# Performance work log

Measured on AMD Instinct MI355X. Metric: run time of the kernel, lower is better.

The kernel has to match this reference:

```python
import jax, jax.numpy as jnp
import numpy as np

N_NODES = 100000
N_EDGES = 1600000
VOCAB = 1000
D_IN = 64
D_H = 128
D_OUT = 1
NEG_SLOPE = 0.2  # PyG GATConv default leaky_relu slope


def setup_inputs() -> dict:
    key = jax.random.key(0)
    ks = jax.random.split(key, 13)
    s_in = 1.0 / np.sqrt(D_IN)
    s_h = 1.0 / np.sqrt(D_H)
    return {
        "x": jax.random.randint(ks[0], (N_NODES,), 0, VOCAB),
        "edge_index": jax.random.randint(ks[1], (2, N_EDGES), 0, N_NODES),
        "node_embeddings": jax.random.normal(ks[2], (VOCAB, D_IN)) * 0.1,
        "W1": jax.random.normal(ks[3], (D_IN, D_H)) * s_in,
        "a_src1": jax.random.normal(ks[4], (D_H,)) * s_h,
        "a_dst1": jax.random.normal(ks[5], (D_H,)) * s_h,
        "b1": jnp.zeros((D_H,)),
        "W2": jax.random.normal(ks[6], (D_H, D_H)) * s_h,
        "a_src2": jax.random.normal(ks[7], (D_H,)) * s_h,
        "a_dst2": jax.random.normal(ks[8], (D_H,)) * s_h,
        "b2": jnp.zeros((D_H,)),
        "W_fc": jax.random.normal(ks[9], (2 * D_H, D_OUT)) * (1.0 / np.sqrt(2 * D_H)),
        "b_fc": jnp.zeros((D_OUT,)),
    }


def segment_softmax(logits, seg, n):
    # numerically-stable softmax over edges grouped by destination node
    mx = jax.ops.segment_max(logits, seg, num_segments=n)
    e = jnp.exp(logits - mx[seg])
    s = jax.ops.segment_sum(e, seg, num_segments=n)
    return e / (s[seg] + 1e-16)


def gat_conv(h, src, dst, W, a_src, a_dst, b):
    # single-head GATConv (PyG defaults: heads=1, negative_slope=0.2, bias)
    h = h @ W                                   # [N, D]
    logit = (h @ a_src)[src] + (h @ a_dst)[dst]  # [E]
    logit = jax.nn.leaky_relu(logit, NEG_SLOPE)
    alpha = segment_softmax(logit, dst, N_NODES)
    out = jax.ops.segment_sum(alpha[:, None] * h[src], dst, num_segments=N_NODES)
    return out + b


def reference(x, edge_index, node_embeddings, W1, a_src1, a_dst1, b1,
              W2, a_src2, a_dst2, b2, W_fc, b_fc):
    h = node_embeddings[x]                      # [N, D_IN]
    src, dst = edge_index[0], edge_index[1]
    # PyG GATConv adds self-loops by default
    loop = jnp.arange(N_NODES)
    src_sl = jnp.concatenate([src, loop])
    dst_sl = jnp.concatenate([dst, loop])
    h = jax.nn.gelu(gat_conv(h, src_sl, dst_sl, W1, a_src1, a_dst1, b1), approximate=False)
    h = jax.nn.gelu(gat_conv(h, src_sl, dst_sl, W2, a_src2, a_dst2, b2), approximate=False)
    # per-edge prediction: concat endpoint features (original edges, no self-loops)
    pair = jnp.concatenate([h[src], h[dst]], axis=-1)   # [E, 2*D_H]
    out = jax.nn.gelu(pair @ W_fc + b_fc, approximate=False)
    return out.squeeze(1)                       # [E]
```

## Files before the change

kernel.cpp:

```cpp
#include <hip/hip_runtime.h>
#include <hip/hip_bf16.h>

#define N_NODES 100000
#define N_EDGES 1600000
#define N_ESL   1700000
#define VOCAB   1000
#define D_IN    64
#define D_H     128
#define NEG_SLOPE 0.2f

#define BSH   7
#define NB    782
#define CAP   3072
#define CHUNK 16384

#define CO_EMB   0
#define CO_W1    64000
#define CO_AS1   72192
#define CO_AD1   72320
#define CO_B1    72448
#define CO_W2    72576
#define CO_AS2   88960
#define CO_AD2   89088
#define CO_B2    89216
#define CO_WFC   89344
#define CO_BFC   89600
#define CO_TOTAL 89601

__device__ __forceinline__ float us2f(unsigned short h){ union{unsigned v; float f;} c; c.v = ((unsigned)h)<<16; return c.f; }
__device__ __forceinline__ float gelu_f(float v){ return 0.5f*v*(1.0f + erff(v*0.7071067811865475f)); }
__device__ __forceinline__ float4 ldf4(const float* p){ return *reinterpret_cast<const float4*>(p); }
__device__ __forceinline__ void stf4(float* p, float4 v){ *reinterpret_cast<float4*>(p) = v; }

__device__ __forceinline__ float wred_sum(float v){
  #pragma unroll
  for (int m=32;m;m>>=1) v += __shfl_xor(v,m,64);
  return v;
}

__global__ __launch_bounds__(64) void k_detect(const unsigned* __restrict__ w, int* __restrict__ flag){
  int t = threadIdx.x;
  float cnt = 0.f;
  #pragma unroll
  for (int i=0;i<2;++i){
    unsigned v = w[t + 64*i];
    unsigned e = (v >> 7) & 0xFFu;
    cnt += (e >= 110u && e <= 126u) ? 1.f : 0.f;
  }
  cnt = wred_sum(cnt);
  if (t==0) *flag = (cnt >= 64.f) ? 1 : 0;
}

__global__ void k_convert(const void* p0, const void* p1, const void* p2, const void* p3,
    const void* p4, const void* p5, const void* p6, const void* p7, const void* p8,
    const void* p9, const void* p10, const int* __restrict__ flag, float* __restrict__ c){
  int i = blockIdx.x*blockDim.x + threadIdx.x;
  if (i >= CO_TOTAL) return;
  const void* src; int off;
  if      (i < CO_W1 ){ src=p0;  off=i;          }
  else if (i < CO_AS1){ src=p1;  off=i-CO_W1;    }
  else if (i < CO_AD1){ src=p2;  off=i-CO_AS1;   }
  else if (i < CO_B1 ){ src=p3;  off=i-CO_AD1;   }
  else if (i < CO_W2 ){ src=p4;  off=i-CO_B1;    }
  else if (i < CO_AS2){ src=p5;  off=i-CO_W2;    }
  else if (i < CO_AD2){ src=p6;  off=i-CO_AS2;   }
  else if (i < CO_B2 ){ src=p7;  off=i-CO_AD2;   }
  else if (i < CO_WFC){ src=p8;  off=i-CO_B2;    }
  else if (i < CO_BFC){ src=p9;  off=i-CO_WFC;   }
  else               { src=p10; off=i-CO_BFC;   }
  float v = (*flag) ? us2f(((const unsigned short*)src)[off]) : ((const float*)src)[off];
  c[i] = v;
}

__global__ __launch_bounds__(256) void k_prevec(const float* __restrict__ cw,
    float* __restrict__ va2, float* __restrict__ vd2){
  int t = threadIdx.x;
  int r = t & 127;
  const float* vec = cw + ((t < 128) ? CO_AS2 : CO_AD2);
  float s = 0.f;
  for (int j=0;j<D_H;++j) s = fmaf(cw[CO_W2 + r*D_H + j], vec[j], s);
  if (t < 128) va2[r] = s; else vd2[r] = s;
}

__global__ __launch_bounds__(64) void k_table1(const float* __restrict__ cw,
    float* __restrict__ table1, float* __restrict__ as1, float* __restrict__ ad1){
  const float* emb = cw + CO_EMB;
  const float* W1  = cw + CO_W1;
  int v = blockIdx.x; int t = threadIdx.x;
  __shared__ float er[D_IN];
  er[t] = emb[v*D_IN + t];
  __syncthreads();
  int d0 = t, d1 = t + 64;
  float a0 = 0.f, a1 = 0.f;
  for (int k=0;k<D_IN;++k){
    float e = er[k];
    a0 = fmaf(e, W1[k*D_H+d0], a0);
    a1 = fmaf(e, W1[k*D_H+d1], a1);
  }
  table1[v*D_H+d0] = a0; table1[v*D_H+d1] = a1;
  float ps = a0*cw[CO_AS1+d0] + a1*cw[CO_AS1+d1];
  float pd = a0*cw[CO_AD1+d0] + a1*cw[CO_AD1+d1];
  ps = wred_sum(ps); pd = wred_sum(pd);
  if (t==0){ as1[v]=ps; ad1[v]=pd; }
}

__global__ void k_nodelog(const int* __restrict__ x, const float* __restrict__ as1,
    const float* __restrict__ ad1, float* __restrict__ sA1, float* __restrict__ dA1){
  int i = blockIdx.x*blockDim.x + threadIdx.x;
  if (i < N_NODES){ int xs = x[i]; sA1[i] = as1[xs]; dA1[i] = ad1[xs]; }
}

__global__ __launch_bounds__(256) void k_bin(const int* __restrict__ src,
    const int* __restrict__ dst, int* __restrict__ gcur, unsigned* __restrict__ ebuf){
  __shared__ int hist[NB];
  __shared__ int cur[NB];
  int tid = threadIdx.x;
  int base0 = blockIdx.x * CHUNK;
  int n = N_ESL - base0; if (n > CHUNK) n = CHUNK;
  for (int i=tid; i<NB; i+=256) hist[i] = 0;
  __syncthreads();
  for (int k=tid; k<n; k+=256){
    int e = base0 + k;
    int d = (e < N_EDGES) ? dst[e] : (e - N_EDGES);
    atomicAdd(&hist[d>>BSH], 1);
  }
  __syncthreads();
  for (int b=tid; b<NB; b+=256){
    int c = hist[b];
    cur[b] = c ? atomicAdd(&gcur[b], c) : 0;
  }
  __syncthreads();
  for (int k=tid; k<n; k+=256){
    int e = base0 + k;
    int s, d;
    if (e < N_EDGES){ s = src[e]; d = dst[e]; } else { s = d = e - N_EDGES; }
    int b = d >> BSH;
    int pos = atomicAdd(&cur[b], 1);
    if (pos < CAP) ebuf[(size_t)b*CAP + pos] = (unsigned)(((d & 127) << 17) | s);
  }
}

__global__ __launch_bounds__(1024) void k_bscan(const int* __restrict__ gcur, int* __restrict__ csrbase){
  int t = threadIdx.x, lane = t & 63, wid = t >> 6;
  int c = (t < NB) ? gcur[t] : 0;
  if (c > CAP) c = CAP;
  int v = c;
  #pragma unroll
  for (int m=1;m<64;m<<=1){ int u = __shfl_up(v,m,64); if (lane>=m) v += u; }
  __shared__ int wsum[16], woff[16];
  if (lane==63) wsum[wid] = v;
  __syncthreads();
  if (t==0){ int run=0; for (int w=0;w<16;++w){ woff[w]=run; run+=wsum[w]; } }
  __syncthreads();
  v += woff[wid];
  if (t < NB) csrbase[t] = v - c;
}

__global__ __launch_bounds__(256) void k_group(const unsigned* __restrict__ ebuf,
    const int* __restrict__ gcur, const int* __restrict__ csrbase,
    int* __restrict__ csr, int* __restrict__ rowoff, int* __restrict__ rowcnt){
  __shared__ unsigned stage[CAP];
  __shared__ int hist[128], lofs[128], cur[128];
  int b = blockIdx.x, tid = threadIdx.x;
  int n = gcur[b]; if (n > CAP) n = CAP;
  int nodeBase = b << BSH;
  int cbase = csrbase[b];
  if (tid < 128) hist[tid] = 0;
  __syncthreads();
  for (int k=tid; k<n; k+=256){
    unsigned p = ebuf[(size_t)b*CAP + k];
    stage[k] = p;
    atomicAdd(&hist[p >> 17], 1);
  }
  __syncthreads();
  if (tid == 0){ int run=0; for (int i=0;i<128;++i){ lofs[i]=run; run+=hist[i]; } }
  __syncthreads();
  if (tid < 128){
    int d = nodeBase + tid;
    if (d < N_NODES){ rowoff[d] = cbase + lofs[tid]; rowcnt[d] = hist[tid]; }
    cur[tid] = lofs[tid];
  }
  __syncthreads();
  for (int k=tid; k<n; k+=256){
    unsigned p = stage[k];
    int pos = atomicAdd(&cur[p >> 17], 1);
    csr[cbase + pos] = (int)(p & 0x1FFFFu);
  }
}

template<int MODE>
__global__ __launch_bounds__(256) void k_agg(const int* __restrict__ rowoff,
    const int* __restrict__ rowcnt, const int* __restrict__ csr_src, const int* __restrict__ x,
    const float* __restrict__ sa, const float* __restrict__ danode,
    const float* __restrict__ feat, const float* __restrict__ cw,
    const float* __restrict__ va2, const float* __restrict__ vd2,
    float* __restrict__ out_h, float* __restrict__ p_lo, float* __restrict__ p_hi){
  int lane = threadIdx.x & 63;
  int node = blockIdx.x*4 + (threadIdx.x >> 6);
  if (node >= N_NODES) return;
  int start = rowoff[node];
  int nj = rowcnt[node];
  int end = start + nj;
  float dA = danode[node];

  float mx, inv;
  float w_sav = 0.f; int rb_sav = 0;
  if (nj <= 64){
    int p = start + lane;
    bool act = p < end;
    int s = 0; float l = -1e30f;
    if (act){
      s = csr_src[p];
      l = sa[s] + dA; l = (l > 0.f) ? l : NEG_SLOPE*l;
      rb_sav = (MODE == 0 ? x[s] : s) * D_H;
    }
    float m = l, ss = act ? 1.0f : 0.0f;
    #pragma unroll
    for (int off=32; off; off>>=1){
      float mo = __shfl_xor(m, off, 64);
      float so = __shfl_xor(ss, off, 64);
      float mn = fmaxf(m, mo);
      ss = ss*expf(m-mn) + so*expf(mo-mn);
      m = mn;
    }
    mx = m; inv = 1.0f/(ss + 1e-16f);
    w_sav = act ? expf(l - mx)*inv : 0.f;
  } else {
    float m = -1e30f, ss = 0.f;
    for (int p = start + lane; p < end; p += 64){
      int s = csr_src[p];
      float l = sa[s] + dA; l = (l > 0.f) ? l : NEG_SLOPE*l;
      float mn = fmaxf(m, l);
      ss = ss*expf(m-mn) + expf(l-mn);
      m = mn;
    }
    #pragma unroll
    for (int off=32; off; off>>=1){
      float mo = __shfl_xor(m, off, 64);
      float so = __shfl_xor(ss, off, 64);
      float mn = fmaxf(m, mo);
      ss = ss*expf(m-mn) + so*expf(mo-mn);
      m = mn;
    }
    mx = m; inv = 1.0f/(ss + 1e-16f);
  }

  int c0 = (lane & 31)*4, half = lane >> 5;
  float a0=0.f, a1=0.f, a2=0.f, a3=0.f;
  for (int t0 = start; t0 < end; t0 += 64){
    float w; int rb;
    if (nj <= 64){ w = w_sav; rb = rb_sav; }
    else {
      int p = t0 + lane;
      w = 0.f; rb = 0;
      if (p < end){
        int s = csr_src[p];
        float l = sa[s] + dA; l = (l > 0.f) ? l : NEG_SLOPE*l;
        w = expf(l - mx)*inv;
        rb = (MODE == 0 ? x[s] : s) * D_H;
      }
    }
    int cnt = end - t0; if (cnt > 64) cnt = 64;
    int mid = (cnt + 1) >> 1;
    int lo = half ? mid : 0;
    int hi = half ? cnt : mid;
    for (int j = lo; j < hi; j += 4){
      int nh = hi - j;
      float w0 = __shfl(w,  j,   64), w1 = __shfl(w,  j+1, 64);
      float w2 = __shfl(w,  j+2, 64), w3 = __shfl(w,  j+3, 64);
      int   r0 = __shfl(rb, j,   64), r1 = __shfl(rb, j+1, 64);
      int   r2 = __shfl(rb, j+2, 64), r3 = __shfl(rb, j+3, 64);
      float4 f0 = make_float4(0.f,0.f,0.f,0.f), f1 = f0, f2 = f0, f3 = f0;
      f0 = ldf4(feat + r0 + c0);
      if (nh > 1) f1 = ldf4(feat + r1 + c0);
      if (nh > 2) f2 = ldf4(feat + r2 + c0);
      if (nh > 3) f3 = ldf4(feat + r3 + c0);
      a0 = fmaf(w0, f0.x, a0); a1 = fmaf(w0, f0.y, a1);
      a2 = fmaf(w0, f0.z, a2); a3 = fmaf(w0, f0.w, a3);
      a0 = fmaf(w1, f1.x, a0); a1 = fmaf(w1, f1.y, a1);
      a2 = fmaf(w1, f1.z, a2); a3 = fmaf(w1, f1.w, a3);
      a0 = fmaf(w2, f2.x, a0); a1 = fmaf(w2, f2.y, a1);
      a2 = fmaf(w2, f2.z, a2); a3 = fmaf(w2, f2.w, a3);
      a0 = fmaf(w3, f3.x, a0); a1 = fmaf(w3, f3.y, a1);
      a2 = fmaf(w3, f3.z, a2); a3 = fmaf(w3, f3.w, a3);
    }
  }
  a0 += __shfl_xor(a0,32,64); a1 += __shfl_xor(a1,32,64);
  a2 += __shfl_xor(a2,32,64); a3 += __shfl_xor(a3,32,64);

  if (MODE == 0){
    float o0 = gelu_f(a0 + cw[CO_B1+c0]);
    float o1 = gelu_f(a1 + cw[CO_B1+c0+1]);
    float o2 = gelu_f(a2 + cw[CO_B1+c0+2]);
    float o3 = gelu_f(a3 + cw[CO_B1+c0+3]);
    if (!half) stf4(out_h + (size_t)node*D_H + c0, make_float4(o0,o1,o2,o3));
    float pl = o0*va2[c0] + o1*va2[c0+1] + o2*va2[c0+2] + o3*va2[c0+3];
    float ph = o0*vd2[c0] + o1*vd2[c0+1] + o2*vd2[c0+2] + o3*vd2[c0+3];
    #pragma unroll
    for (int off=16; off; off>>=1){ pl += __shfl_xor(pl,off,64); ph += __shfl_xor(ph,off,64); }
    if (lane == 0){ p_lo[node] = pl; p_hi[node] = ph; }
  } else if (MODE == 1){
    if (!half) stf4(out_h + (size_t)node*D_H + c0, make_float4(a0,a1,a2,a3));
  } else {
    float o0 = gelu_f(a0 + cw[CO_B2+c0]);
    float o1 = gelu_f(a1 + cw[CO_B2+c0+1]);
    float o2 = gelu_f(a2 + cw[CO_B2+c0+2]);
    float o3 = gelu_f(a3 + cw[CO_B2+c0+3]);
    float pl = o0*cw[CO_WFC+c0]     + o1*cw[CO_WFC+c0+1]
             + o2*cw[CO_WFC+c0+2]   + o3*cw[CO_WFC+c0+3];
    float ph = o0*cw[CO_WFC+D_H+c0]   + o1*cw[CO_WFC+D_H+c0+1]
             + o2*cw[CO_WFC+D_H+c0+2] + o3*cw[CO_WFC+D_H+c0+3];
    #pragma unroll
    for (int off=16; off; off>>=1){ pl += __shfl_xor(pl,off,64); ph += __shfl_xor(ph,off,64); }
    if (lane == 0){ p_lo[node] = pl; p_hi[node] = ph; }
  }
}

__global__ __launch_bounds__(256) void k_post(const float* __restrict__ agg2,
    const float* __restrict__ cw, float* __restrict__ p_lo, float* __restrict__ p_hi){
  const float* W2 = cw + CO_W2;
  __shared__ float xr[16][D_H];
  __shared__ float cws[4][8][2];
  int tid = threadIdx.x;
  int col = tid & 127, half = tid >> 7, wid = tid >> 6;
  int base = blockIdx.x * 64;
  float wlo = cw[CO_WFC+col], whi = cw[CO_WFC+D_H+col], b2 = cw[CO_B2+col];
  for (int t0=0; t0<64; t0+=16){
    int r0 = base + t0;
    for (int i=tid; i<16*D_H; i+=256){
      int rr = r0 + (i>>7);
      xr[i>>7][i&127] = (rr < N_NODES) ? agg2[(size_t)rr*D_H + (i&127)] : 0.f;
    }
    __syncthreads();
    float acc[8];
    #pragma unroll
    for (int r=0;r<8;++r) acc[r] = 0.f;
    int rb = half*8;
    for (int k=0;k<D_H;++k){
      float wv = W2[k*D_H + col];
      #pragma unroll
      for (int r=0;r<8;++r) acc[r] = fmaf(xr[rb+r][k], wv, acc[r]);
    }
    #pragma unroll
    for (int r=0;r<8;++r){
      float o = gelu_f(acc[r] + b2);
      float ps = wred_sum(o*wlo);
      float pd = wred_sum(o*whi);
      if ((tid & 63)==0){ cws[wid][r][0]=ps; cws[wid][r][1]=pd; }
    }
    __syncthreads();
    if (tid < 16){
      int hh = tid>>3, r = tid&7, rr = r0 + hh*8 + r;
      if (rr < N_NODES){
        p_lo[rr] = cws[hh*2][r][0] + cws[hh*2+1][r][0];
        p_hi[rr] = cws[hh*2][r][1] + cws[hh*2+1][r][1];
      }
    }
    __syncthreads();
  }
}

__global__ __launch_bounds__(256) void k_matmul2(float* __restrict__ hbuf, const float* __restrict__ cw){
  const float* W2 = cw + CO_W2;
  __shared__ float xr[16][D_H];
  int tid = threadIdx.x;
  int col = tid & 127, half = tid >> 7;
  int base = blockIdx.x * 64;
  for (int t0=0; t0<64; t0+=16){
    int r0 = base + t0;
    for (int i=tid; i<16*D_H; i+=256){
      int rr = r0 + (i>>7);
      xr[i>>7][i&127] = (rr < N_NODES) ? hbuf[(size_t)rr*D_H + (i&127)] : 0.f;
    }
    __syncthreads();
    float acc[8];
    #pragma unroll
    for (int r=0;r<8;++r) acc[r] = 0.f;
    int rb = half*8;
    for (int k=0;k<D_H;++k){
      float wv = W2[k*D_H + col];
      #pragma unroll
      for (int r=0;r<8;++r) acc[r] = fmaf(xr[rb+r][k], wv, acc[r]);
    }
    #pragma unroll
    for (int r=0;r<8;++r){
      int rr = r0 + rb + r;
      if (rr < N_NODES) hbuf[(size_t)rr*D_H + col] = acc[r];
    }
    __syncthreads();
  }
}

__global__ void k_final(const int* __restrict__ src, const int* __restrict__ dst,
    const float* __restrict__ p_lo, const float* __restrict__ p_hi,
    const float* __restrict__ cw, const int* __restrict__ flag, void* __restrict__ out){
  int q = blockIdx.x*blockDim.x + threadIdx.x;
  int e0 = q*4;
  if (e0 >= N_EDGES) return;
  float bfc = cw[CO_BFC];
  if (e0 + 4 <= N_EDGES){
    int4 s4 = *reinterpret_cast<const int4*>(src + e0);
    int4 d4 = *reinterpret_cast<const int4*>(dst + e0);
    float4 v;
    v.x = gelu_f(p_lo[s4.x] + p_hi[d4.x] + bfc);
    v.y = gelu_f(p_lo[s4.y] + p_hi[d4.y] + bfc);
    v.z = gelu_f(p_lo[s4.z] + p_hi[d4.z] + bfc);
    v.w = gelu_f(p_lo[s4.w] + p_hi[d4.w] + bfc);
    if (*flag){
      __hip_bfloat16* o = (__hip_bfloat16*)out + e0;
      o[0]=__float2bfloat16(v.x); o[1]=__float2bfloat16(v.y);
      o[2]=__float2bfloat16(v.z); o[3]=__float2bfloat16(v.w);
    } else {
      stf4((float*)out + e0, v);
    }
  } else {
    for (int e = e0; e < N_EDGES; ++e){
      float v = gelu_f(p_lo[src[e]] + p_hi[dst[e]] + bfc);
      if (*flag) ((__hip_bfloat16*)out)[e] = __float2bfloat16(v);
      else       ((float*)out)[e] = v;
    }
  }
}

extern "C" void kernel_launch(void* const* d_in, const int* in_sizes, int n_in,
                              void* d_out, int out_size, void* d_ws, size_t ws_size,
                              hipStream_t stream){
  (void)in_sizes; (void)n_in; (void)out_size;
  const int* x  = (const int*)d_in[0];
  const int* ei = (const int*)d_in[1];
  const int* src = ei;
  const int* dst = ei + N_EDGES;

  char* base = (char*)d_ws;
  size_t off = 0;
  auto A = [&](size_t bytes)->size_t{ size_t r = off; off = (off + bytes + 255) & ~(size_t)255; return r; };
  size_t o_flag   = A(4);
  size_t o_cw     = A((size_t)CO_TOTAL*4);
  size_t o_va2    = A(D_H*4);
  size_t o_vd2    = A(D_H*4);
  size_t o_table1 = A((size_t)VOCAB*D_H*4);
  size_t o_as1    = A(VOCAB*4);
  size_t o_ad1    = A(VOCAB*4);
  size_t o_sA1    = A((size_t)N_NODES*4);
  size_t o_dA1    = A((size_t)N_NODES*4);
  size_t o_sA2    = A((size_t)N_NODES*4);
  size_t o_dA2    = A((size_t)N_NODES*4);
  size_t o_rowoff = A((size_t)N_NODES*4);
  size_t o_rowcnt = A((size_t)N_NODES*4);
  size_t o_plo    = A((size_t)N_NODES*4);
  size_t o_phi    = A((size_t)N_NODES*4);
  size_t o_gcur   = A((size_t)NB*4);
  size_t o_cbase  = A((size_t)NB*4);
  size_t o_csr    = A((size_t)N_ESL*4);
  size_t o_big    = A((size_t)N_NODES*D_H*4);
  size_t need_b   = off;
  size_t o_agg2   = A((size_t)N_NODES*D_H*4);
  size_t need_a   = off;

  int*   flag   = (int*)(base + o_flag);
  float* cw     = (float*)(base + o_cw);
  float* va2    = (float*)(base + o_va2);
  float* vd2    = (float*)(base + o_vd2);
  float* table1 = (float*)(base + o_table1);
  float* as1    = (float*)(base + o_as1);
  float* ad1    = (float*)(base + o_ad1);
  float* sA1    = (float*)(base + o_sA1);
  float* dA1    = (float*)(base + o_dA1);
  float* sA2    = (float*)(base + o_sA2);
  float* dA2    = (float*)(base + o_dA2);
  int*   rowoff = (int*)(base + o_rowoff);
  int*   rowcnt = (int*)(base + o_rowcnt);
  float* plo    = (float*)(base + o_plo);
  float* phi    = (float*)(base + o_phi);
  int*   gcur   = (int*)(base + o_gcur);
  int*   cbase  = (int*)(base + o_cbase);
  int*   csr    = (int*)(base + o_csr);
  float* hbuf   = (float*)(base + o_big);
  unsigned* ebuf= (unsigned*)(base + o_big);
  float* agg2   = (float*)(base + o_agg2);

  if (ws_size < need_b) return;
  bool patha = (ws_size >= need_a);

  k_detect<<<1, 64, 0, stream>>>((const unsigned*)d_in[2], flag);
  k_convert<<<(CO_TOTAL+255)/256, 256, 0, stream>>>(d_in[2], d_in[3], d_in[4], d_in[5],
      d_in[6], d_in[7], d_in[8], d_in[9], d_in[10], d_in[11], d_in[12], flag, cw);
  k_prevec<<<1, 256, 0, stream>>>(cw, va2, vd2);
  k_table1<<<VOCAB, 64, 0, stream>>>(cw, table1, as1, ad1);
  k_nodelog<<<(N_NODES+255)/256, 256, 0, stream>>>(x, as1, ad1, sA1, dA1);

  hipMemsetAsync(gcur, 0, (size_t)NB*4, stream);
  k_bin<<<(N_ESL+CHUNK-1)/CHUNK, 256, 0, stream>>>(src, dst, gcur, ebuf);
  k_bscan<<<1, 1024, 0, stream>>>(gcur, cbase);
  k_group<<<NB, 256, 0, stream>>>(ebuf, gcur, cbase, csr, rowoff, rowcnt);

  int nagg = (N_NODES+3)/4;
  k_agg<0><<<nagg, 256, 0, stream>>>(rowoff, rowcnt, csr, x, sA1, dA1, table1, cw, va2, vd2, hbuf, sA2, dA2);
  if (patha){
    k_agg<1><<<nagg, 256, 0, stream>>>(rowoff, rowcnt, csr, x, sA2, dA2, hbuf, cw, va2, vd2, agg2, nullptr, nullptr);
    k_post<<<(N_NODES+63)/64, 256, 0, stream>>>(agg2, cw, plo, phi);
  } else {
    k_matmul2<<<(N_NODES+63)/64, 256, 0, stream>>>(hbuf, cw);
    k_agg<2><<<nagg, 256, 0, stream>>>(rowoff, rowcnt, csr, x, sA2, dA2, hbuf, cw, va2, vd2, nullptr, plo, phi);
  }
  k_final<<<(N_EDGES/4+255)/256, 256, 0, stream>>>(src, dst, plo, phi, cw, flag, d_out);
}
```

Before: 431.8 us.

## Register-tile k_post matmul with shared W2 tiles and float4 accumulators

```diff
diff --git a/kernel.cpp b/kernel.cpp
--- a/kernel.cpp
+++ b/kernel.cpp
@@ -318,45 +318,62 @@
 
 __global__ __launch_bounds__(256) void k_post(const float* __restrict__ agg2,
     const float* __restrict__ cw, float* __restrict__ p_lo, float* __restrict__ p_hi){
+  __shared__ float xr[64][D_H];
+  __shared__ float W[64][D_H];
   const float* W2 = cw + CO_W2;
-  __shared__ float xr[16][D_H];
-  __shared__ float cws[4][8][2];
   int tid = threadIdx.x;
-  int col = tid & 127, half = tid >> 7, wid = tid >> 6;
+  int cg = tid & 31;
+  int rg = tid >> 5;
   int base = blockIdx.x * 64;
-  float wlo = cw[CO_WFC+col], whi = cw[CO_WFC+D_H+col], b2 = cw[CO_B2+col];
-  for (int t0=0; t0<64; t0+=16){
-    int r0 = base + t0;
-    for (int i=tid; i<16*D_H; i+=256){
-      int rr = r0 + (i>>7);
-      xr[i>>7][i&127] = (rr < N_NODES) ? agg2[(size_t)rr*D_H + (i&127)] : 0.f;
-    }
+
+  for (int i = tid; i < 64*D_H/4; i += 256){
+    int row = i >> 5, c4 = (i & 31) * 4;
+    int rr = base + row;
+    float4 v = (rr < N_NODES) ? ldf4(agg2 + (size_t)rr*D_H + c4) : make_float4(0.f,0.f,0.f,0.f);
+    stf4(&xr[row][c4], v);
+  }
+
+  float4 acc[8];
+  #pragma unroll
+  for (int rs=0; rs<8; ++rs) acc[rs] = make_float4(0.f,0.f,0.f,0.f);
+
+  #pragma unroll
+  for (int hk = 0; hk < 2; ++hk){
     __syncthreads();
-    float acc[8];
-    #pragma unroll
-    for (int r=0;r<8;++r) acc[r] = 0.f;
-    int rb = half*8;
-    for (int k=0;k<D_H;++k){
-      float wv = W2[k*D_H + col];
+    for (int i = tid; i < 64*D_H/4; i += 256){
+      int k = i >> 5, c4 = (i & 31) * 4;
+      stf4(&W[k][c4], ldf4(W2 + (size_t)(hk*64 + k)*D_H + c4));
+    }
+    __syncthreads();
+    for (int k = 0; k < 64; ++k){
+      float4 wv = ldf4(&W[k][cg*4]);
+      int kk = hk*64 + k;
       #pragma unroll
-      for (int r=0;r<8;++r) acc[r] = fmaf(xr[rb+r][k], wv, acc[r]);
-    }
-    #pragma unroll
-    for (int r=0;r<8;++r){
-      float o = gelu_f(acc[r] + b2);
-      float ps = wred_sum(o*wlo);
-      float pd = wred_sum(o*whi);
-      if ((tid & 63)==0){ cws[wid][r][0]=ps; cws[wid][r][1]=pd; }
-    }
-    __syncthreads();
-    if (tid < 16){
-      int hh = tid>>3, r = tid&7, rr = r0 + hh*8 + r;
-      if (rr < N_NODES){
-        p_lo[rr] = cws[hh*2][r][0] + cws[hh*2+1][r][0];
-        p_hi[rr] = cws[hh*2][r][1] + cws[hh*2+1][r][1];
+      for (int rs = 0; rs < 8; ++rs){
+        float xv = xr[rs*8 + rg][kk];
+        acc[rs].x = fmaf(xv, wv.x, acc[rs].x);
+        acc[rs].y = fmaf(xv, wv.y, acc[rs].y);
+        acc[rs].z = fmaf(xv, wv.z, acc[rs].z);
+        acc[rs].w = fmaf(xv, wv.w, acc[rs].w);
       }
     }
-    __syncthreads();
+  }
+
+  float4 b2v = ldf4(cw + CO_B2  + cg*4);
+  float4 wlo = ldf4(cw + CO_WFC + cg*4);
+  float4 whi = ldf4(cw + CO_WFC + D_H + cg*4);
+  #pragma unroll
+  for (int rs = 0; rs < 8; ++rs){
+    int rr = base + rs*8 + rg;
+    float o0 = gelu_f(acc[rs].x + b2v.x);
+    float o1 = gelu_f(acc[rs].y + b2v.y);
+    float o2 = gelu_f(acc[rs].z + b2v.z);
+    float o3 = gelu_f(acc[rs].w + b2v.w);
+    float pl = o0*wlo.x + o1*wlo.y + o2*wlo.z + o3*wlo.w;
+    float ph = o0*whi.x + o1*whi.y + o2*whi.z + o3*whi.w;
+    #pragma unroll
+    for (int off=16; off; off>>=1){ pl += __shfl_xor(pl,off,64); ph += __shfl_xor(ph,off,64); }
+    if (cg == 0 && rr < N_NODES){ p_lo[rr] = pl; p_hi[rr] = ph; }
   }
 }
 
```

After: 382.0 us. 11.5% less time.
